# Performance work log

Hardware: AMD Instinct MI355X
Metric: run time of the kernel (lower is better)

The kernel has to match this reference:

```python
import jax, jax.numpy as jnp
import numpy as np

N_BATCH, D_FEAT, N_CLASSES = 96, 64, 21
MARGIN = 0.3


def setup_inputs() -> dict:
    key = jax.random.key(0)
    k1, k2, k3 = jax.random.split(key, 3)
    logits = jax.random.normal(k1, (N_BATCH, D_FEAT), dtype=jnp.float32)
    feat2 = jax.random.normal(k2, (N_BATCH, D_FEAT), dtype=jnp.float32)
    labels = (jax.random.uniform(k3, (N_BATCH, N_CLASSES)) < 0.3).astype(jnp.float32)
    return {"logits": logits, "labels": labels, "feat2": feat2}


def reference(logits, labels, feat2):
    """Dense-mask formulation of QuadrupletMarginMiner (defaults:
    margin=0.3, type_of_quadruplets='all', what_is_hard='one').

    Instead of a data-dependent list of quadruplets, returns a boolean
    tensor valid[i, j, k, n] that is True exactly for the quadruplets the
    torch module would return (same set, dense encoding).
    """
    n = labels.shape[0]
    eps = 1e-12

    # --- label structure ------------------------------------------------
    s = (labels @ labels.T) > 0                      # share-a-label matrix
    diffs = ~s                                       # torch: sames ^ 1 (pre diag fill)
    sames = s & ~jnp.eye(n, dtype=bool)              # fill_diagonal_(0)
    jk_triu = jnp.triu(jnp.ones((n, n), dtype=bool), k=1)  # strict j < k

    # valid (I, J, K) triples: AP1 & AP2 & j<k   -> [n, n, n]
    triple = sames[:, :, None] & sames[:, None, :] & jk_triu[None, :, :]
    # attach every negative N: diffs[i, n]        -> [n, n, n, n]
    quad = triple[:, :, :, None] & diffs[:, None, None, :]

    # --- distances (negative cosine similarity) ---------------------------
    xn = logits / jnp.maximum(jnp.linalg.norm(logits, axis=1, keepdims=True), eps)
    yn = feat2 / jnp.maximum(jnp.linalg.norm(feat2, axis=1, keepdims=True), eps)
    mat = -(xn @ yn.T)                               # [n, n]

    # margin_p[i, p, neg] = mat[i, neg] - mat[i, p]  (p stands for J or K)
    margin_pn = mat[:, None, :] - mat[:, :, None]    # [i, p, neg]
    viol = margin_pn <= MARGIN                       # [i, p, neg] bool

    # 'all' quadruplets + 'one' hardness: (margin1 <= m) | (margin2 <= m)
    cond = viol[:, :, None, :] | viol[:, None, :, :]  # [i, j, k, neg]

    return quad & cond
```

## Files before the change

kernel.cpp:

```cpp
#include <hip/hip_runtime.h>
#include <math.h>

#define NB 96
#define NB2 (NB * NB)
#define DFEAT 64
#define NCLS 21
#define MARGIN 0.3

typedef int i4 __attribute__((ext_vector_type(4)));

__global__ __launch_bounds__(384) void fused_quad_kernel(
    const float* __restrict__ logits,
    const float* __restrict__ labels,
    const float* __restrict__ feat2,
    int* __restrict__ out) {
  const int bid = blockIdx.x;
  const int i = bid / NB;
  const int j = bid - i * NB;
  const int tid = threadIdx.x;

  __shared__ double smat[NB];
  __shared__ double sthr[NB];
  __shared__ unsigned char svalid[NB];

  {
    const int n = tid >> 2;
    const int l4 = tid & 3;
    const float* xi = logits + i * DFEAT + l4 * 16;
    const float* yn = feat2 + n * DFEAT + l4 * 16;
    double dot = 0.0, nx = 0.0, ny = 0.0;
#pragma unroll
    for (int d = 0; d < 16; ++d) {
      double a = (double)xi[d];
      double b = (double)yn[d];
      dot += a * b;
      nx += a * a;
      ny += b * b;
    }
    dot += __shfl_xor(dot, 1); nx += __shfl_xor(nx, 1); ny += __shfl_xor(ny, 1);
    dot += __shfl_xor(dot, 2); nx += __shfl_xor(nx, 2); ny += __shfl_xor(ny, 2);
    if (l4 == 0) {
      nx = fmax(sqrt(nx), 1e-12);
      ny = fmax(sqrt(ny), 1e-12);
      double m = -(dot / (nx * ny));
      const float* li = labels + i * NCLS;
      const float* ln = labels + n * NCLS;
      float ld = 0.f;
#pragma unroll
      for (int c = 0; c < NCLS; ++c) ld += li[c] * ln[c];
      const bool share = (ld > 0.f);
      smat[n] = share ? 1e300 : m;
      sthr[n] = MARGIN + m;
      svalid[n] = (share && n != i) ? 1 : 0;
    }
  }
  __syncthreads();

  const bool sames_ij = (svalid[j] != 0);
  const double thr_ij = sthr[j];
  i4* outp = (i4*)(out + (size_t)bid * (size_t)NB2);

  const int q = tid % 24;
  const int kg = tid / 24;
  const int n0 = q * 4;
  const double d0 = smat[n0 + 0];
  const double d1 = smat[n0 + 1];
  const double d2 = smat[n0 + 2];
  const double d3 = smat[n0 + 3];

#pragma unroll
  for (int r = 0; r < 6; ++r) {
    const int k = kg * 6 + r;
    i4 v = (i4)(0);
    if (sames_ij && svalid[k] && (j < k)) {
      const double t = fmax(thr_ij, sthr[k]);
      v.x = (d0 <= t) ? 1 : 0;
      v.y = (d1 <= t) ? 1 : 0;
      v.z = (d2 <= t) ? 1 : 0;
      v.w = (d3 <= t) ? 1 : 0;
    }
    __builtin_nontemporal_store(v, &outp[k * 24 + q]);
  }
}

extern "C" void kernel_launch(void* const* d_in, const int* in_sizes, int n_in,
                              void* d_out, int out_size, void* d_ws, size_t ws_size,
                              hipStream_t stream) {
  const float* logits = (const float*)d_in[0];
  const float* labels = (const float*)d_in[1];
  const float* feat2  = (const float*)d_in[2];
  int* out = (int*)d_out;

  fused_quad_kernel<<<NB2, 384, 0, stream>>>(logits, labels, feat2, out);
}
```

Measured before the change: 339.5 us.

## Process four j per block and precompute violation bitmasks

Each block now handles four j values for one i, which cuts the grid by four and spreads the per-block prologue (cosine distances, label overlap) over four times as much output. Per-k violation masks are precomputed as 32-bit words in shared memory and ORed per (j,k), so the store loop only extracts bits. The nontemporal store hint is dropped in favour of plain stores, which changes cache behaviour for the large output write.

```diff
diff --git a/kernel.cpp b/kernel.cpp
--- a/kernel.cpp
+++ b/kernel.cpp
@@ -6,6 +6,9 @@
 #define DFEAT 64
 #define NCLS 21
 #define MARGIN 0.3
+#define JPB 4
+#define NJB (NB / JPB)
+#define NBLK (NB * NJB)
 
 typedef int i4 __attribute__((ext_vector_type(4)));
 
@@ -15,13 +18,15 @@
     const float* __restrict__ feat2,
     int* __restrict__ out) {
   const int bid = blockIdx.x;
-  const int i = bid / NB;
-  const int j = bid - i * NB;
+  const int i = bid / NJB;
+  const int j4 = (bid - i * NJB) * JPB;
   const int tid = threadIdx.x;
 
   __shared__ double smat[NB];
   __shared__ double sthr[NB];
   __shared__ unsigned char svalid[NB];
+  __shared__ unsigned int bits[NB][3];
+  __shared__ unsigned int gw[JPB][NB][3];
 
   {
     const int n = tid >> 2;
@@ -56,30 +61,50 @@
   }
   __syncthreads();
 
-  const bool sames_ij = (svalid[j] != 0);
-  const double thr_ij = sthr[j];
-  i4* outp = (i4*)(out + (size_t)bid * (size_t)NB2);
+  if (tid < NB * 3) {
+    const int k = tid / 3;
+    const int w = tid - 3 * k;
+    const double t = sthr[k];
+    unsigned int m = 0u;
+#pragma unroll
+    for (int b = 0; b < 32; ++b)
+      m |= (smat[w * 32 + b] <= t) ? (1u << b) : 0u;
+    bits[k][w] = m;
+  }
+  __syncthreads();
+
+#pragma unroll
+  for (int s = 0; s < 3; ++s) {
+    const int u = tid + s * 384;
+    const int jj = u / (NB * 3);
+    const int rem = u - jj * (NB * 3);
+    const int k = rem / 3;
+    const int w = rem - 3 * k;
+    const int j = j4 + jj;
+    const bool gate = svalid[j] && svalid[k] && (j < k);
+    gw[jj][k][w] = gate ? (bits[j][w] | bits[k][w]) : 0u;
+  }
+  __syncthreads();
 
   const int q = tid % 24;
-  const int kg = tid / 24;
-  const int n0 = q * 4;
-  const double d0 = smat[n0 + 0];
-  const double d1 = smat[n0 + 1];
-  const double d2 = smat[n0 + 2];
-  const double d3 = smat[n0 + 3];
+  const int kr = tid / 24;
+  const int wi = q >> 3;
+  const int bb = (q & 7) * 4;
+  i4* outp = (i4*)(out + (size_t)(i * NB + j4) * (size_t)NB2);
 
 #pragma unroll
-  for (int r = 0; r < 6; ++r) {
-    const int k = kg * 6 + r;
-    i4 v = (i4)(0);
-    if (sames_ij && svalid[k] && (j < k)) {
-      const double t = fmax(thr_ij, sthr[k]);
-      v.x = (d0 <= t) ? 1 : 0;
-      v.y = (d1 <= t) ? 1 : 0;
-      v.z = (d2 <= t) ? 1 : 0;
-      v.w = (d3 <= t) ? 1 : 0;
+  for (int jj = 0; jj < JPB; ++jj) {
+#pragma unroll
+    for (int r = 0; r < 6; ++r) {
+      const int k = 16 * r + kr;
+      const unsigned int wv = gw[jj][k][wi];
+      i4 v;
+      v.x = (int)((wv >> bb) & 1u);
+      v.y = (int)((wv >> (bb + 1)) & 1u);
+      v.z = (int)((wv >> (bb + 2)) & 1u);
+      v.w = (int)((wv >> (bb + 3)) & 1u);
+      outp[jj * (NB2 / 4) + k * 24 + q] = v;
     }
-    __builtin_nontemporal_store(v, &outp[k * 24 + q]);
   }
 }
 
@@ -91,5 +116,5 @@
   const float* feat2  = (const float*)d_in[2];
   int* out = (int*)d_out;
 
-  fused_quad_kernel<<<NB2, 384, 0, stream>>>(logits, labels, feat2, out);
+  fused_quad_kernel<<<NBLK, 384, 0, stream>>>(logits, labels, feat2, out);
 }
```

Result: slower. 346.8 us (+2.2%).

## Precompute violation bitmasks per (i,p) and stream output from compact tables

Applied to the files above, without the earlier changes.

Splits the fused kernel into two. A small table kernel computes the distance row once per anchor i and packs the violation comparisons into 96-bit masks per (i,p), plus a validity byte table. A grid-stride streaming kernel then expands those masks into the dense int output with nontemporal vector stores. The original recomputed the 64-dim dot products in double for every (i,j) block, 96x redundantly. The cost is an extra launch, a workspace round trip, and integer div/mod per element in the store loop.

```diff
diff --git a/kernel.cpp b/kernel.cpp
--- a/kernel.cpp
+++ b/kernel.cpp
@@ -9,19 +9,18 @@
 
 typedef int i4 __attribute__((ext_vector_type(4)));
 
-__global__ __launch_bounds__(384) void fused_quad_kernel(
+
+__global__ __launch_bounds__(384) void table_kernel(
     const float* __restrict__ logits,
     const float* __restrict__ labels,
     const float* __restrict__ feat2,
-    int* __restrict__ out) {
-  const int bid = blockIdx.x;
-  const int i = bid / NB;
-  const int j = bid - i * NB;
+    unsigned int* __restrict__ bitsT,
+    unsigned char* __restrict__ svalT) {
+  const int i = blockIdx.x;
   const int tid = threadIdx.x;
 
   __shared__ double smat[NB];
   __shared__ double sthr[NB];
-  __shared__ unsigned char svalid[NB];
 
   {
     const int n = tid >> 2;
@@ -51,35 +50,54 @@
       const bool share = (ld > 0.f);
       smat[n] = share ? 1e300 : m;
       sthr[n] = MARGIN + m;
-      svalid[n] = (share && n != i) ? 1 : 0;
+      svalT[i * NB + n] = (share && n != i) ? 1 : 0;
     }
   }
   __syncthreads();
 
-  const bool sames_ij = (svalid[j] != 0);
-  const double thr_ij = sthr[j];
-  i4* outp = (i4*)(out + (size_t)bid * (size_t)NB2);
+  if (tid < NB * 3) {
+    const int x = tid / 3;
+    const int w = tid - 3 * x;
+    const double t = sthr[x];
+    unsigned int m = 0u;
+#pragma unroll
+    for (int b = 0; b < 32; ++b)
+      m |= (smat[w * 32 + b] <= t) ? (1u << b) : 0u;
+    bitsT[(i * NB + x) * 3 + w] = m;
+  }
+}
 
-  const int q = tid % 24;
-  const int kg = tid / 24;
-  const int n0 = q * 4;
-  const double d0 = smat[n0 + 0];
-  const double d1 = smat[n0 + 1];
-  const double d2 = smat[n0 + 2];
-  const double d3 = smat[n0 + 3];
+#define TOT4 (NB * NB2 * 24)
+#define SBLK 2592
 
-#pragma unroll
-  for (int r = 0; r < 6; ++r) {
-    const int k = kg * 6 + r;
-    i4 v = (i4)(0);
-    if (sames_ij && svalid[k] && (j < k)) {
-      const double t = fmax(thr_ij, sthr[k]);
-      v.x = (d0 <= t) ? 1 : 0;
-      v.y = (d1 <= t) ? 1 : 0;
-      v.z = (d2 <= t) ? 1 : 0;
-      v.w = (d3 <= t) ? 1 : 0;
-    }
-    __builtin_nontemporal_store(v, &outp[k * 24 + q]);
+__global__ __launch_bounds__(256) void stream_kernel(
+    const unsigned int* __restrict__ bitsT,
+    const unsigned char* __restrict__ svalT,
+    int* __restrict__ out) {
+  const unsigned int stride = SBLK * 256;
+  unsigned int f = blockIdx.x * 256 + threadIdx.x;
+  i4* outp = (i4*)out;
+#pragma unroll 4
+  for (int it = 0; it < 32; ++it, f += stride) {
+    const unsigned int row = f / 24u;
+    const unsigned int q = f - row * 24u;
+    const unsigned int ij = row / 96u;
+    const unsigned int k = row - ij * 96u;
+    const unsigned int i = ij / 96u;
+    const unsigned int j = ij - i * 96u;
+    const unsigned int ik = ij - j + k;
+    const unsigned int w = q >> 3;
+    const unsigned int g =
+        (unsigned int)(svalT[ij] & svalT[ik]) & (unsigned int)(j < k);
+    const unsigned int wv =
+        (bitsT[ij * 3u + w] | bitsT[ik * 3u + w]) & (0u - g);
+    const unsigned int bb = (q & 7u) * 4u;
+    i4 v;
+    v.x = (int)((wv >> bb) & 1u);
+    v.y = (int)((wv >> (bb + 1u)) & 1u);
+    v.z = (int)((wv >> (bb + 2u)) & 1u);
+    v.w = (int)((wv >> (bb + 3u)) & 1u);
+    __builtin_nontemporal_store(v, &outp[f]);
   }
 }
 
@@ -91,5 +109,9 @@
   const float* feat2  = (const float*)d_in[2];
   int* out = (int*)d_out;
 
-  fused_quad_kernel<<<NB2, 384, 0, stream>>>(logits, labels, feat2, out);
+  unsigned int* bitsT = (unsigned int*)d_ws;
+  unsigned char* svalT = (unsigned char*)(bitsT + NB2 * 3);
+
+  table_kernel<<<NB, 384, 0, stream>>>(logits, labels, feat2, bitsT, svalT);
+  stream_kernel<<<SBLK, 256, 0, stream>>>(bitsT, svalT, out);
 }
```

After: 341.4 us. About the same (+0.6%).
